# Kernel optimization log

Hardware: AMD Instinct MI355X
Metric: run time of the kernel (lower is better)

## Reference

```python
import jax, jax.numpy as jnp
import numpy as np

HEADS = 8
DIM_HEAD = 64


def setup_inputs() -> dict:
    key = jax.random.key(0)
    k1, k2, k3 = jax.random.split(key, 3)
    dim_in = 256
    hidden = HEADS * DIM_HEAD  # 512
    x = jax.random.normal(k1, (2, dim_in, 64, 64), dtype=jnp.float32)
    # 1x1 conv weights stored as [out_ch, in_ch]
    w_qkv = jax.random.normal(k2, (3 * hidden, dim_in), dtype=jnp.float32) * (1.0 / np.sqrt(dim_in))
    w_out = jax.random.normal(k3, (dim_in, hidden), dtype=jnp.float32) * (1.0 / np.sqrt(hidden))
    b_out = jnp.zeros((dim_in,), dtype=jnp.float32)
    return {"x": x, "w_qkv": w_qkv, "w_out": w_out, "b_out": b_out}


def reference(x, w_qkv, w_out, b_out):
    b, c, H, W = x.shape
    S = H * W
    scale = 1.0 / np.sqrt(DIM_HEAD)
    # 1x1 conv == per-pixel linear projection
    qkv = jnp.einsum('bcxy,oc->boxy', x, w_qkv)  # [b, 3*hidden, H, W]
    q, k, v = jnp.split(qkv, 3, axis=1)
    # 'b (h c) x y -> b h c (x y)'
    def to_heads(z):
        return z.reshape(b, HEADS, DIM_HEAD, S)
    q = to_heads(q) * scale
    k = to_heads(k)
    v = to_heads(v)
    sim = jnp.einsum('bhdi,bhdj->bhij', q, k)  # [b, h, S, S]
    sim = sim - jax.lax.stop_gradient(jnp.max(sim, axis=-1, keepdims=True))
    attn = jax.nn.softmax(sim, axis=-1)
    out = jnp.einsum('bhij,bhdj->bhid', attn, v)  # [b, h, S, d]
    # 'b h (x y) d -> b (h d) x y'
    out = out.transpose(0, 1, 3, 2).reshape(b, HEADS * DIM_HEAD, H, W)
    return jnp.einsum('bcxy,oc->boxy', out, w_out) + b_out[None, :, None, None]
```

## Files before the change

kernel.cpp:

```cpp
#include <hip/hip_runtime.h>
#include <cmath>

#define S_TOT 4096
#define CIN   256
#define HID   512
#define NHEAD 8
#define DIMH  64

typedef __attribute__((ext_vector_type(8))) short bf16x8;
typedef __attribute__((ext_vector_type(4))) float f32x4;
typedef __attribute__((ext_vector_type(16))) float f32x16;
typedef __attribute__((address_space(1))) const void gv_t;
typedef __attribute__((address_space(3))) void lv_t;

__device__ __forceinline__ ushort f2bf(float f) {
    union { float f; unsigned u; } v; v.f = f;
    unsigned r = (v.u + 0x7FFFu + ((v.u >> 16) & 1u)) >> 16;
    return (ushort)r;
}

__device__ __forceinline__ float bf2f(ushort u) {
    union { unsigned u; float f; } v; v.u = ((unsigned)u) << 16; return v.f;
}

__device__ __forceinline__ float exp2_fast(float x) {
    float r; asm("v_exp_f32 %0, %1" : "=v"(r) : "v"(x)); return r;
}

__device__ __forceinline__ unsigned cvt_pk_bf16(float lo, float hi) {
    unsigned r; asm("v_cvt_pk_bf16_f32 %0, %1, %2" : "=v"(r) : "v"(lo), "v"(hi)); return r;
}

#define QSCALE 0.18033688011112042f

__global__ __launch_bounds__(256)
void prologue_kernel(const float* __restrict__ w_qkv, const float* __restrict__ w_out,
                     const float* __restrict__ x, ushort* __restrict__ wqb,
                     ushort* __restrict__ wob, ushort* __restrict__ xt) {
    __shared__ float tb[64][65];
    const int bid = blockIdx.x, t = threadIdx.x;
    if (bid < 512) {
        const float* src = (bid < 384) ? w_qkv : w_out;
        ushort* dst = (bid < 384) ? wqb : wob;
        const long i = ((long)(bid < 384 ? bid : bid - 384) * 256 + t) * 4;
        float4 v = *(const float4*)&src[i];
        ushort4 p;
        p.x = f2bf(v.x); p.y = f2bf(v.y); p.z = f2bf(v.z); p.w = f2bf(v.w);
        *(ushort4*)&dst[i] = p;
        return;
    }
    const int xb_ = bid - 512;
    const int sx = xb_ & 63, rest = xb_ >> 6;
    const int cy = rest & 3, cz = rest >> 2;
    const int s0 = sx * 64, c0 = cy * 64;
    const long xb = (long)cz * CIN * S_TOT;
    #pragma unroll
    for (int i = 0; i < 16; ++i) {
        int idx = t + i * 256;
        int c = idx >> 6, s = idx & 63;
        tb[c][s] = x[xb + (long)(c0 + c) * S_TOT + s0 + s];
    }
    __syncthreads();
    const long ob = (long)cz * S_TOT * CIN;
    const int s = t >> 2, cq = (t & 3) * 16;
    #pragma unroll
    for (int j = 0; j < 4; ++j) {
        ushort4 pk;
        pk.x = f2bf(tb[cq + j * 4 + 0][s]);
        pk.y = f2bf(tb[cq + j * 4 + 1][s]);
        pk.z = f2bf(tb[cq + j * 4 + 2][s]);
        pk.w = f2bf(tb[cq + j * 4 + 3][s]);
        *(ushort4*)&xt[ob + (long)(s0 + s) * CIN + c0 + cq + j * 4] = pk;
    }
}

template<int MODE>
__global__ __launch_bounds__(256)
void gemm_mfma_kernel(const ushort* __restrict__ Ag, const ushort* __restrict__ Bg,
                      void* __restrict__ outp, const float* __restrict__ bias,
                      int Kdim, long strideA, long strideB) {
    __shared__ __attribute__((aligned(16))) ushort Abuf[128 * 64];
    __shared__ __attribute__((aligned(16))) ushort Bbuf[128 * 64];
    const int t = threadIdx.x, lane = t & 63;
    const int l15 = lane & 15, g = lane >> 4;
    const int wid = t >> 6, wr = wid >> 1, wc = wid & 1;
    const int bz = blockIdx.z;
    const int am0 = blockIdx.y * 128, bn0 = blockIdx.x * 128;
    Ag += (long)bz * strideA;
    Bg += (long)bz * strideB;

    f32x4 acc[4][4];
    #pragma unroll
    for (int i = 0; i < 4; ++i)
        #pragma unroll
        for (int j = 0; j < 4; ++j)
            acc[i][j] = (f32x4){0.f, 0.f, 0.f, 0.f};

    for (int k0 = 0; k0 < Kdim; k0 += 64) {
        __syncthreads();
        #pragma unroll
        for (int i = 0; i < 4; ++i) {
            const int chunk = t + i * 256;
            const int row = chunk >> 3, sl = chunk & 7;
            const ushort* srcA = Ag + (long)(am0 + row) * Kdim + k0 + ((sl ^ (row & 7)) << 3);
            __builtin_amdgcn_global_load_lds((gv_t*)srcA,
                (lv_t*)((char*)Abuf + (i * 256 + (t & ~63)) * 16), 16, 0, 0);
            const ushort* srcB = Bg + (long)(bn0 + row) * Kdim + k0 + ((sl ^ (row & 7)) << 3);
            __builtin_amdgcn_global_load_lds((gv_t*)srcB,
                (lv_t*)((char*)Bbuf + (i * 256 + (t & ~63)) * 16), 16, 0, 0);
        }
        asm volatile("s_waitcnt vmcnt(0)" ::: "memory");
        __syncthreads();

        bf16x8 bfr[4][2];
        #pragma unroll
        for (int fn = 0; fn < 4; ++fn) {
            const int row = wc * 64 + fn * 16 + l15;
            #pragma unroll
            for (int hf = 0; hf < 2; ++hf)
                bfr[fn][hf] = *(const bf16x8*)((const char*)Bbuf + row * 128
                                + (((hf * 4 + g) ^ (row & 7)) << 4));
        }
        #pragma unroll
        for (int fm = 0; fm < 4; ++fm) {
            const int row = wr * 64 + fm * 16 + l15;
            const bf16x8 a0 = *(const bf16x8*)((const char*)Abuf + row * 128
                                + (((g) ^ (row & 7)) << 4));
            const bf16x8 a1 = *(const bf16x8*)((const char*)Abuf + row * 128
                                + (((4 + g) ^ (row & 7)) << 4));
            #pragma unroll
            for (int fn = 0; fn < 4; ++fn) {
                acc[fm][fn] = __builtin_amdgcn_mfma_f32_16x16x32_bf16(a0, bfr[fn][0], acc[fm][fn], 0, 0, 0);
                acc[fm][fn] = __builtin_amdgcn_mfma_f32_16x16x32_bf16(a1, bfr[fn][1], acc[fm][fn], 0, 0, 0);
            }
        }
    }

    #pragma unroll
    for (int fm = 0; fm < 4; ++fm)
        #pragma unroll
        for (int fn = 0; fn < 4; ++fn)
            #pragma unroll
            for (int r = 0; r < 4; ++r) {
                const int ar = am0 + wr * 64 + fm * 16 + g * 4 + r;
                const int bc = bn0 + wc * 64 + fn * 16 + l15;
                if (MODE == 0) {
                    const int which = bc >> 9, h = (bc >> 6) & 7, d = bc & 63;
                    const float scl = (which == 0) ? QSCALE : 1.0f;
                    ushort* O = (ushort*)outp;
                    O[(long)which * 4194304 + (((long)(bz * NHEAD + h)) * S_TOT + ar) * DIMH + d]
                        = f2bf(acc[fm][fn][r] * scl);
                } else if (MODE == 1) {
                    const int h = ar >> 6, d = ar & 63;
                    const int jm = bc & 15;
                    const int pjm = (jm & 3) | ((jm & 4) << 1) | ((jm & 8) >> 1);
                    const int pc = (bc & ~15) | pjm;
                    ushort* O = (ushort*)outp;
                    O[(((long)(bz * NHEAD + h)) * DIMH + d) * S_TOT + pc] = f2bf(acc[fm][fn][r]);
                } else {
                    float* O = (float*)outp;
                    O[((long)bz * CIN + ar) * S_TOT + bc] = acc[fm][fn][r] + bias[ar];
                }
            }
}

__global__ __launch_bounds__(256, 4)
void attn_mfma_kernel(const ushort* __restrict__ qg, const ushort* __restrict__ kg,
                      const ushort* __restrict__ vg, ushort* __restrict__ pout,
                      float2* __restrict__ mlout) {
    __shared__ __attribute__((aligned(16))) ushort kbuf[2][64 * 64];
    __shared__ __attribute__((aligned(16))) ushort vbuf[2][64 * 64];

    const int t = threadIdx.x;
    const int lane = t & 63, wid = t >> 6;
    const int l31 = lane & 31, h = lane >> 5;
    const int head = blockIdx.y;
    const int b = blockIdx.z >> 1, sp = blockIdx.z & 1;
    const int bh = b * NHEAD + head;
    const int qrow0 = blockIdx.x * 128 + wid * 32;
    const long kbase = (long)sp * (S_TOT / 2);

    const int sw_lo = (l31 ^ (l31 >> 3)) & 7;
    const int sw_hi = sw_lo ^ 4;

    const ushort* qp = qg + ((long)bh * S_TOT + qrow0 + l31) * DIMH + h * 8;
    bf16x8 qfr[4];
    #pragma unroll
    for (int ds = 0; ds < 4; ++ds) qfr[ds] = *(const bf16x8*)(qp + ds * 16);

    f32x16 oacc0 = {}, oacc1 = {};
    f32x16 bias16 = {};
    float nmr = 0.f, lrun = 0.f;

    const long kg_base = (long)bh * S_TOT * DIMH;
    const long vg_base = (long)bh * DIMH * S_TOT;
    const int sl = lane & 7, sr = lane >> 3;

    auto STAGE = [&](int buf, long key0) {
        #pragma unroll
        for (int c = 0; c < 2; ++c) {
            const int row = wid * 16 + c * 8 + sr;
            const int sz = (sl ^ sr ^ (wid * 2 + c)) & 7;
            char* kdst = (char*)(&kbuf[buf][0]) + wid * 2048 + c * 1024;
            char* vdst = (char*)(&vbuf[buf][0]) + wid * 2048 + c * 1024;
            const char* srcK = (const char*)(kg + kg_base + (key0 + row) * DIMH) + (sz << 4);
            __builtin_amdgcn_global_load_lds((gv_t*)srcK, (lv_t*)kdst, 16, 0, 0);
            const char* srcV = (const char*)(vg + vg_base + (long)row * S_TOT + key0) + (sz << 4);
            __builtin_amdgcn_global_load_lds((gv_t*)srcV, (lv_t*)vdst, 16, 0, 0);
        }
    };

    STAGE(0, kbase);
    asm volatile("s_waitcnt vmcnt(0)" ::: "memory");
    __syncthreads();

    const int NT = (S_TOT / 2) / 64;
    for (int kt0 = 0; kt0 < NT; ++kt0) {
        const int cur = kt0 & 1;
        if (kt0 + 1 < NT) STAGE(cur ^ 1, kbase + (long)(kt0 + 1) * 64);

        const char* kb_ = (const char*)(&kbuf[cur][0]);
        const char* vb_ = (const char*)(&vbuf[cur][0]);

        f32x16 s0, s1;
        __builtin_amdgcn_s_setprio(1);
        {
            const bf16x8 kf0 = *(const bf16x8*)(kb_ + l31 * 128 + ((h ^ sw_lo) << 4));
            const bf16x8 kf1 = *(const bf16x8*)(kb_ + 4096 + l31 * 128 + ((h ^ sw_hi) << 4));
            s0 = __builtin_amdgcn_mfma_f32_32x32x16_bf16(kf0, qfr[0], bias16, 0, 0, 0);
            s1 = __builtin_amdgcn_mfma_f32_32x32x16_bf16(kf1, qfr[0], bias16, 0, 0, 0);
        }
        #pragma unroll
        for (int ds = 1; ds < 4; ++ds) {
            const bf16x8 kf0 = *(const bf16x8*)(kb_ + l31 * 128 + (((2 * ds + h) ^ sw_lo) << 4));
            const bf16x8 kf1 = *(const bf16x8*)(kb_ + 4096 + l31 * 128 + (((2 * ds + h) ^ sw_hi) << 4));
            s0 = __builtin_amdgcn_mfma_f32_32x32x16_bf16(kf0, qfr[ds], s0, 0, 0, 0);
            s1 = __builtin_amdgcn_mfma_f32_32x32x16_bf16(kf1, qfr[ds], s1, 0, 0, 0);
        }
        __builtin_amdgcn_s_setprio(0);

        bf16x8 pf0, pf1, pf2, pf3;
        {
            float e[16];
            #pragma unroll
            for (int r = 0; r < 16; ++r) e[r] = exp2_fast(s0[r]);
            #pragma unroll
            for (int r = 0; r < 16; ++r) lrun += e[r];
            union { unsigned u[4]; bf16x8 v; } A_, B_;
            #pragma unroll
            for (int w = 0; w < 4; ++w) A_.u[w] = cvt_pk_bf16(e[2 * w], e[2 * w + 1]);
            #pragma unroll
            for (int w = 0; w < 4; ++w) B_.u[w] = cvt_pk_bf16(e[8 + 2 * w], e[9 + 2 * w]);
            pf0 = A_.v; pf1 = B_.v;
        }
        {
            float e[16];
            #pragma unroll
            for (int r = 0; r < 16; ++r) e[r] = exp2_fast(s1[r]);
            #pragma unroll
            for (int r = 0; r < 16; ++r) lrun += e[r];
            union { unsigned u[4]; bf16x8 v; } A_, B_;
            #pragma unroll
            for (int w = 0; w < 4; ++w) A_.u[w] = cvt_pk_bf16(e[2 * w], e[2 * w + 1]);
            #pragma unroll
            for (int w = 0; w < 4; ++w) B_.u[w] = cvt_pk_bf16(e[8 + 2 * w], e[9 + 2 * w]);
            pf2 = A_.v; pf3 = B_.v;
        }

        __builtin_amdgcn_s_setprio(1);
        {
            const bf16x8 vf00 = *(const bf16x8*)(vb_ + l31 * 128 + ((h ^ sw_lo) << 4));
            const bf16x8 vf01 = *(const bf16x8*)(vb_ + 4096 + l31 * 128 + ((h ^ sw_hi) << 4));
            oacc0 = __builtin_amdgcn_mfma_f32_32x32x16_bf16(pf0, vf00, oacc0, 0, 0, 0);
            oacc1 = __builtin_amdgcn_mfma_f32_32x32x16_bf16(pf0, vf01, oacc1, 0, 0, 0);
            const bf16x8 vf10 = *(const bf16x8*)(vb_ + l31 * 128 + (((2 + h) ^ sw_lo) << 4));
            const bf16x8 vf11 = *(const bf16x8*)(vb_ + 4096 + l31 * 128 + (((2 + h) ^ sw_hi) << 4));
            oacc0 = __builtin_amdgcn_mfma_f32_32x32x16_bf16(pf1, vf10, oacc0, 0, 0, 0);
            oacc1 = __builtin_amdgcn_mfma_f32_32x32x16_bf16(pf1, vf11, oacc1, 0, 0, 0);
            const bf16x8 vf20 = *(const bf16x8*)(vb_ + l31 * 128 + (((4 + h) ^ sw_lo) << 4));
            const bf16x8 vf21 = *(const bf16x8*)(vb_ + 4096 + l31 * 128 + (((4 + h) ^ sw_hi) << 4));
            oacc0 = __builtin_amdgcn_mfma_f32_32x32x16_bf16(pf2, vf20, oacc0, 0, 0, 0);
            oacc1 = __builtin_amdgcn_mfma_f32_32x32x16_bf16(pf2, vf21, oacc1, 0, 0, 0);
            const bf16x8 vf30 = *(const bf16x8*)(vb_ + l31 * 128 + (((6 + h) ^ sw_lo) << 4));
            const bf16x8 vf31 = *(const bf16x8*)(vb_ + 4096 + l31 * 128 + (((6 + h) ^ sw_hi) << 4));
            oacc0 = __builtin_amdgcn_mfma_f32_32x32x16_bf16(pf3, vf30, oacc0, 0, 0, 0);
            oacc1 = __builtin_amdgcn_mfma_f32_32x32x16_bf16(pf3, vf31, oacc1, 0, 0, 0);
        }
        __builtin_amdgcn_s_setprio(0);

        if (__any(lrun > 1.6777216e7f)) {
            const float sc = 5.9604644775390625e-8f;
            lrun *= sc;
            #pragma unroll
            for (int r = 0; r < 16; ++r) { oacc0[r] *= sc; oacc1[r] *= sc; }
            nmr -= 24.0f;
            #pragma unroll
            for (int r = 0; r < 16; ++r) bias16[r] = nmr;
        }

        asm volatile("s_waitcnt vmcnt(0)" ::: "memory");
        __syncthreads();
    }

    lrun += __shfl_xor(lrun, 32, 64);
    const long pbase = (((long)sp * 2 + b) * S_TOT) * HID;
    #pragma unroll
    for (int r = 0; r < 16; ++r) {
        const int q = (r & 3) + 8 * (r >> 2) + 4 * h;
        const long off = pbase + (long)(qrow0 + q) * HID + head * 64 + l31;
        pout[off]      = f2bf(oacc0[r]);
        pout[off + 32] = f2bf(oacc1[r]);
    }
    if (h == 0)
        mlout[((long)sp * 2 * NHEAD * S_TOT) + (long)bh * S_TOT + qrow0 + l31]
            = make_float2(-nmr, lrun);
}

__global__ __launch_bounds__(256)
void attn_merge_kernel(const ushort* __restrict__ part, const float2* __restrict__ ml,
                       ushort* __restrict__ aout) {
    const long i = (long)blockIdx.x * 256 + threadIdx.x;
    const int hd8 = (int)(i & 63);
    const long bq = i >> 6;
    const int q = (int)(bq & (S_TOT - 1)), b = (int)(bq >> 12);
    const int h = hd8 >> 3;
    const long mlst = (long)2 * NHEAD * S_TOT;
    const float2 ml0 = ml[(long)(b * NHEAD + h) * S_TOT + q];
    const float2 ml1 = ml[mlst + (long)(b * NHEAD + h) * S_TOT + q];
    const float m = fmaxf(ml0.x, ml1.x);
    const float w0 = exp2_fast(ml0.x - m), w1 = exp2_fast(ml1.x - m);
    const float inv = 1.0f / (w0 * ml0.y + w1 * ml1.y);
    const long phalf = (long)2 * S_TOT * HID;
    const long off = ((long)b * S_TOT + q) * HID + hd8 * 8;
    const bf16x8 p0 = *(const bf16x8*)&part[off];
    const bf16x8 p1 = *(const bf16x8*)&part[phalf + off];
    union { ushort u[8]; bf16x8 v; } o;
    #pragma unroll
    for (int j = 0; j < 8; ++j)
        o.u[j] = f2bf((w0 * bf2f((ushort)p0[j]) + w1 * bf2f((ushort)p1[j])) * inv);
    *(bf16x8*)&aout[off] = o.v;
}

extern "C" void kernel_launch(void* const* d_in, const int* in_sizes, int n_in,
                              void* d_out, int out_size, void* d_ws, size_t ws_size,
                              hipStream_t stream) {
    const float* x     = (const float*)d_in[0];
    const float* w_qkv = (const float*)d_in[1];
    const float* w_out = (const float*)d_in[2];
    const float* b_out = (const float*)d_in[3];
    float* out = (float*)d_out;

    const long PERQKV = (long)2 * NHEAD * S_TOT * DIMH;
    ushort* qws = (ushort*)d_ws;
    ushort* kws = qws + PERQKV;
    ushort* vws = kws + PERQKV;
    ushort* xt  = vws + PERQKV;
    ushort* wqb = xt + (long)2 * S_TOT * CIN;
    ushort* wob = wqb + (long)3 * HID * CIN;
    ushort* awb = wob + (long)CIN * HID;
    ushort* prt = awb + (long)2 * S_TOT * HID;
    float2* mlw = (float2*)(prt + (long)4 * S_TOT * HID);

    prologue_kernel<<<dim3(1024), 256, 0, stream>>>(w_qkv, w_out, x, wqb, wob, xt);

    gemm_mfma_kernel<0><<<dim3(1024 / 128, S_TOT / 128, 2), 256, 0, stream>>>(
        xt, wqb, qws, nullptr, CIN, (long)S_TOT * CIN, 0L);
    gemm_mfma_kernel<1><<<dim3(S_TOT / 128, 512 / 128, 2), 256, 0, stream>>>(
        wqb + (long)1024 * CIN, xt, vws, nullptr, CIN, 0L, (long)S_TOT * CIN);

    attn_mfma_kernel<<<dim3(S_TOT / 128, NHEAD, 4), 256, 0, stream>>>(
        qws, kws, vws, prt, mlw);
    attn_merge_kernel<<<dim3((2 * S_TOT * 64) / 256), 256, 0, stream>>>(prt, mlw, awb);

    gemm_mfma_kernel<2><<<dim3(S_TOT / 128, CIN / 128, 2), 256, 0, stream>>>(
        wob, awb, out, b_out, HID, 0L, (long)S_TOT * HID);
}
```

Before: 122.3 us.

## Fuse QK and V projection GEMMs into one launch and merge into output GEMM

```diff
diff --git a/kernel.cpp b/kernel.cpp
--- a/kernel.cpp
+++ b/kernel.cpp
@@ -74,20 +74,22 @@
     }
 }
 
-template<int MODE>
 __global__ __launch_bounds__(256)
-void gemm_mfma_kernel(const ushort* __restrict__ Ag, const ushort* __restrict__ Bg,
-                      void* __restrict__ outp, const float* __restrict__ bias,
-                      int Kdim, long strideA, long strideB) {
+void gemm_qkv_kernel(const ushort* __restrict__ xt, const ushort* __restrict__ wqb,
+                     ushort* __restrict__ qkws, ushort* __restrict__ vws) {
     __shared__ __attribute__((aligned(16))) ushort Abuf[128 * 64];
     __shared__ __attribute__((aligned(16))) ushort Bbuf[128 * 64];
     const int t = threadIdx.x, lane = t & 63;
     const int l15 = lane & 15, g = lane >> 4;
     const int wid = t >> 6, wr = wid >> 1, wc = wid & 1;
-    const int bz = blockIdx.z;
-    const int am0 = blockIdx.y * 128, bn0 = blockIdx.x * 128;
-    Ag += (long)bz * strideA;
-    Bg += (long)bz * strideB;
+
+    const int bid = blockIdx.x;
+    int mode, bx, by, bz;
+    if (bid < 512) { mode = 0; bx = bid & 7;  by = (bid >> 3) & 31; bz = bid >> 8; }
+    else { const int id = bid - 512; mode = 1; bx = id & 31; by = (id >> 5) & 3; bz = id >> 7; }
+    const int am0 = by * 128, bn0 = bx * 128;
+    const ushort* Ag = (mode == 0) ? (xt + (long)bz * S_TOT * CIN) : (wqb + (long)1024 * CIN);
+    const ushort* Bg = (mode == 0) ? wqb : (xt + (long)bz * S_TOT * CIN);
 
     f32x4 acc[4][4];
     #pragma unroll
@@ -96,16 +98,16 @@
         for (int j = 0; j < 4; ++j)
             acc[i][j] = (f32x4){0.f, 0.f, 0.f, 0.f};
 
-    for (int k0 = 0; k0 < Kdim; k0 += 64) {
+    for (int k0 = 0; k0 < CIN; k0 += 64) {
         __syncthreads();
         #pragma unroll
         for (int i = 0; i < 4; ++i) {
             const int chunk = t + i * 256;
             const int row = chunk >> 3, sl = chunk & 7;
-            const ushort* srcA = Ag + (long)(am0 + row) * Kdim + k0 + ((sl ^ (row & 7)) << 3);
+            const ushort* srcA = Ag + (long)(am0 + row) * CIN + k0 + ((sl ^ (row & 7)) << 3);
             __builtin_amdgcn_global_load_lds((gv_t*)srcA,
                 (lv_t*)((char*)Abuf + (i * 256 + (t & ~63)) * 16), 16, 0, 0);
-            const ushort* srcB = Bg + (long)(bn0 + row) * Kdim + k0 + ((sl ^ (row & 7)) << 3);
+            const ushort* srcB = Bg + (long)(bn0 + row) * CIN + k0 + ((sl ^ (row & 7)) << 3);
             __builtin_amdgcn_global_load_lds((gv_t*)srcB,
                 (lv_t*)((char*)Bbuf + (i * 256 + (t & ~63)) * 16), 16, 0, 0);
         }
@@ -144,22 +146,17 @@
             for (int r = 0; r < 4; ++r) {
                 const int ar = am0 + wr * 64 + fm * 16 + g * 4 + r;
                 const int bc = bn0 + wc * 64 + fn * 16 + l15;
-                if (MODE == 0) {
+                if (mode == 0) {
                     const int which = bc >> 9, h = (bc >> 6) & 7, d = bc & 63;
                     const float scl = (which == 0) ? QSCALE : 1.0f;
-                    ushort* O = (ushort*)outp;
-                    O[(long)which * 4194304 + (((long)(bz * NHEAD + h)) * S_TOT + ar) * DIMH + d]
+                    qkws[(long)which * 4194304 + (((long)(bz * NHEAD + h)) * S_TOT + ar) * DIMH + d]
                         = f2bf(acc[fm][fn][r] * scl);
-                } else if (MODE == 1) {
+                } else {
                     const int h = ar >> 6, d = ar & 63;
                     const int jm = bc & 15;
                     const int pjm = (jm & 3) | ((jm & 4) << 1) | ((jm & 8) >> 1);
                     const int pc = (bc & ~15) | pjm;
-                    ushort* O = (ushort*)outp;
-                    O[(((long)(bz * NHEAD + h)) * DIMH + d) * S_TOT + pc] = f2bf(acc[fm][fn][r]);
-                } else {
-                    float* O = (float*)outp;
-                    O[((long)bz * CIN + ar) * S_TOT + bc] = acc[fm][fn][r] + bias[ar];
+                    vws[(((long)(bz * NHEAD + h)) * DIMH + d) * S_TOT + pc] = f2bf(acc[fm][fn][r]);
                 }
             }
 }
@@ -317,28 +314,97 @@
 }
 
 __global__ __launch_bounds__(256)
-void attn_merge_kernel(const ushort* __restrict__ part, const float2* __restrict__ ml,
-                       ushort* __restrict__ aout) {
-    const long i = (long)blockIdx.x * 256 + threadIdx.x;
-    const int hd8 = (int)(i & 63);
-    const long bq = i >> 6;
-    const int q = (int)(bq & (S_TOT - 1)), b = (int)(bq >> 12);
-    const int h = hd8 >> 3;
-    const long mlst = (long)2 * NHEAD * S_TOT;
-    const float2 ml0 = ml[(long)(b * NHEAD + h) * S_TOT + q];
-    const float2 ml1 = ml[mlst + (long)(b * NHEAD + h) * S_TOT + q];
-    const float m = fmaxf(ml0.x, ml1.x);
-    const float w0 = exp2_fast(ml0.x - m), w1 = exp2_fast(ml1.x - m);
-    const float inv = 1.0f / (w0 * ml0.y + w1 * ml1.y);
-    const long phalf = (long)2 * S_TOT * HID;
-    const long off = ((long)b * S_TOT + q) * HID + hd8 * 8;
-    const bf16x8 p0 = *(const bf16x8*)&part[off];
-    const bf16x8 p1 = *(const bf16x8*)&part[phalf + off];
-    union { ushort u[8]; bf16x8 v; } o;
-    #pragma unroll
-    for (int j = 0; j < 8; ++j)
-        o.u[j] = f2bf((w0 * bf2f((ushort)p0[j]) + w1 * bf2f((ushort)p1[j])) * inv);
-    *(bf16x8*)&aout[off] = o.v;
+void gemm_out_merge_kernel(const ushort* __restrict__ Ag, const ushort* __restrict__ part,
+                           const float2* __restrict__ ml, float* __restrict__ outp,
+                           const float* __restrict__ bias) {
+    __shared__ __attribute__((aligned(16))) ushort Abuf[128 * 64];
+    __shared__ __attribute__((aligned(16))) ushort Bbuf[128 * 64];
+    const int t = threadIdx.x, lane = t & 63;
+    const int l15 = lane & 15, g = lane >> 4;
+    const int wid = t >> 6, wr = wid >> 1, wc = wid & 1;
+    const int bz = blockIdx.z;
+    const int am0 = blockIdx.y * 128, bn0 = blockIdx.x * 128;
+    const long PSP = (long)2 * S_TOT * HID;
+    const long MLSP = (long)2 * NHEAD * S_TOT;
+
+    f32x4 acc[4][4];
+    #pragma unroll
+    for (int i = 0; i < 4; ++i)
+        #pragma unroll
+        for (int j = 0; j < 4; ++j)
+            acc[i][j] = (f32x4){0.f, 0.f, 0.f, 0.f};
+
+    for (int k0 = 0; k0 < HID; k0 += 64) {
+        __syncthreads();
+        #pragma unroll
+        for (int i = 0; i < 4; ++i) {
+            const int chunk = t + i * 256;
+            const int row = chunk >> 3, sl = chunk & 7;
+            const ushort* srcA = Ag + (long)(am0 + row) * HID + k0 + ((sl ^ (row & 7)) << 3);
+            __builtin_amdgcn_global_load_lds((gv_t*)srcA,
+                (lv_t*)((char*)Abuf + (i * 256 + (t & ~63)) * 16), 16, 0, 0);
+        }
+        const int h = k0 >> 6;
+        const long mlb = (long)(bz * NHEAD + h) * S_TOT;
+        #pragma unroll
+        for (int i = 0; i < 4; ++i) {
+            const int chunk = t + i * 256;
+            const int row = chunk >> 3, sl = chunk & 7;
+            const int s = bn0 + row;
+            const float2 ml0 = ml[mlb + s];
+            const float2 ml1 = ml[MLSP + mlb + s];
+            const float m = fmaxf(ml0.x, ml1.x);
+            const float w0 = exp2_fast(ml0.x - m), w1 = exp2_fast(ml1.x - m);
+            const float inv = 1.0f / (w0 * ml0.y + w1 * ml1.y);
+            const long off = ((long)bz * S_TOT + s) * HID + k0 + ((sl ^ (row & 7)) << 3);
+            const bf16x8 p0 = *(const bf16x8*)&part[off];
+            const bf16x8 p1 = *(const bf16x8*)&part[PSP + off];
+            union { unsigned u[4]; bf16x8 v; } M_;
+            #pragma unroll
+            for (int w = 0; w < 4; ++w) {
+                const float e0 = (w0 * bf2f((ushort)p0[2 * w])     + w1 * bf2f((ushort)p1[2 * w]))     * inv;
+                const float e1 = (w0 * bf2f((ushort)p0[2 * w + 1]) + w1 * bf2f((ushort)p1[2 * w + 1])) * inv;
+                M_.u[w] = cvt_pk_bf16(e0, e1);
+            }
+            *(bf16x8*)((char*)Bbuf + (long)chunk * 16) = M_.v;
+        }
+        asm volatile("s_waitcnt vmcnt(0)" ::: "memory");
+        __syncthreads();
+
+        bf16x8 bfr[4][2];
+        #pragma unroll
+        for (int fn = 0; fn < 4; ++fn) {
+            const int row = wc * 64 + fn * 16 + l15;
+            #pragma unroll
+            for (int hf = 0; hf < 2; ++hf)
+                bfr[fn][hf] = *(const bf16x8*)((const char*)Bbuf + row * 128
+                                + (((hf * 4 + g) ^ (row & 7)) << 4));
+        }
+        #pragma unroll
+        for (int fm = 0; fm < 4; ++fm) {
+            const int row = wr * 64 + fm * 16 + l15;
+            const bf16x8 a0 = *(const bf16x8*)((const char*)Abuf + row * 128
+                                + (((g) ^ (row & 7)) << 4));
+            const bf16x8 a1 = *(const bf16x8*)((const char*)Abuf + row * 128
+                                + (((4 + g) ^ (row & 7)) << 4));
+            #pragma unroll
+            for (int fn = 0; fn < 4; ++fn) {
+                acc[fm][fn] = __builtin_amdgcn_mfma_f32_16x16x32_bf16(a0, bfr[fn][0], acc[fm][fn], 0, 0, 0);
+                acc[fm][fn] = __builtin_amdgcn_mfma_f32_16x16x32_bf16(a1, bfr[fn][1], acc[fm][fn], 0, 0, 0);
+            }
+        }
+    }
+
+    #pragma unroll
+    for (int fm = 0; fm < 4; ++fm)
+        #pragma unroll
+        for (int fn = 0; fn < 4; ++fn)
+            #pragma unroll
+            for (int r = 0; r < 4; ++r) {
+                const int ar = am0 + wr * 64 + fm * 16 + g * 4 + r;
+                const int bc = bn0 + wc * 64 + fn * 16 + l15;
+                outp[((long)bz * CIN + ar) * S_TOT + bc] = acc[fm][fn][r] + bias[ar];
+            }
 }
 
 extern "C" void kernel_launch(void* const* d_in, const int* in_sizes, int n_in,
@@ -363,15 +429,11 @@
 
     prologue_kernel<<<dim3(1024), 256, 0, stream>>>(w_qkv, w_out, x, wqb, wob, xt);
 
-    gemm_mfma_kernel<0><<<dim3(1024 / 128, S_TOT / 128, 2), 256, 0, stream>>>(
-        xt, wqb, qws, nullptr, CIN, (long)S_TOT * CIN, 0L);
-    gemm_mfma_kernel<1><<<dim3(S_TOT / 128, 512 / 128, 2), 256, 0, stream>>>(
-        wqb + (long)1024 * CIN, xt, vws, nullptr, CIN, 0L, (long)S_TOT * CIN);
+    gemm_qkv_kernel<<<dim3(768), 256, 0, stream>>>(xt, wqb, qws, vws);
 
     attn_mfma_kernel<<<dim3(S_TOT / 128, NHEAD, 4), 256, 0, stream>>>(
         qws, kws, vws, prt, mlw);
-    attn_merge_kernel<<<dim3((2 * S_TOT * 64) / 256), 256, 0, stream>>>(prt, mlw, awb);
-
-    gemm_mfma_kernel<2><<<dim3(S_TOT / 128, CIN / 128, 2), 256, 0, stream>>>(
-        wob, awb, out, b_out, HID, 0L, (long)S_TOT * HID);
-}
+
+    gemm_out_merge_kernel<<<dim3(S_TOT / 128, CIN / 128, 2), 256, 0, stream>>>(
+        wob, prt, mlw, out, b_out);
+}
```

New measurement: 120.2 us (median of 2 runs). No clear change (-1.8%).
